# Kernel tuning notes

Measured on AMD Instinct MI355X. Metric: run time of the kernel, lower is better.

The kernel has to match this reference:

```python
import jax, jax.numpy as jnp
import numpy as np

E = 8          # moe_expert_count
CAPACITY = 1024  # per-expert capacity C = S / E (capacity factor 1)


def _top1_gate(features, wg):
    """Top-1 gate with capacity, returning combine_weights [S,E,C],
    dispatch_mask [S,E,C], and load-balancing aux loss (standard Switch/BASE-style gate
    matching the (l_aux, combine_weights, dispatch_mask) interface used by BaseLayer)."""
    S, M = features.shape
    logits = features @ wg                      # [S, E]
    gates = jax.nn.softmax(logits, axis=-1)     # [S, E]
    idx = jnp.argmax(gates, axis=-1)            # [S] expert assignment
    mask1 = jax.nn.one_hot(idx, E, dtype=features.dtype)  # [S, E]
    # position of each token inside its expert's buffer (0-based, order of arrival)
    locations = jnp.cumsum(mask1, axis=0) - mask1          # [S, E]
    loc = jnp.sum(locations * mask1, axis=1).astype(jnp.int32)  # [S]
    keep = (loc < CAPACITY).astype(features.dtype)          # drop overflow tokens
    mask1 = mask1 * keep[:, None]
    gate_s = jnp.sum(gates * mask1, axis=1)                 # [S] gate prob of kept tokens
    loc_oh = jax.nn.one_hot(loc, CAPACITY, dtype=features.dtype)  # [S, C]
    combine = gate_s[:, None, None] * mask1[:, :, None] * loc_oh[:, None, :]  # [S,E,C]
    dispatch = (combine > 0).astype(features.dtype)
    # load-balance aux loss: E * sum(mean_prob_e * frac_tokens_e)
    me = jnp.mean(gates, axis=0)
    ce = jnp.mean(mask1, axis=0)
    l_aux = jnp.sum(me * ce) * E
    return l_aux, combine, dispatch


def setup_inputs() -> dict:
    key = jax.random.key(0)
    k0, k1, k2, k3 = jax.random.split(key, 4)
    B, T, M, H = 4, 2048, 512, 1024
    return {
        "hidden_states": jax.random.normal(k0, (B, T, M), dtype=jnp.float32),
        "wg": jax.random.normal(k1, (M, E), dtype=jnp.float32) * 0.02,
        "w1": jax.random.normal(k2, (E, M, H), dtype=jnp.float32) * 0.02,
        "b1": jnp.zeros((E, H), dtype=jnp.float32),
        "w2": jax.random.normal(k3, (E, H, M), dtype=jnp.float32) * 0.02,
        "b2": jnp.zeros((E, M), dtype=jnp.float32),
    }


def reference(hidden_states, wg, w1, b1, w2, b2):
    B, T, M = hidden_states.shape
    feats = hidden_states.reshape(-1, M)            # [S, M]
    l_aux, combine, dispatch = _top1_gate(feats, wg)
    # dense one-hot dispatch matmul: (E*C, S) @ (S, M) -> [E, C, M]
    dispatched = jnp.einsum('sec,sm->ecm', dispatch, feats)
    # per-expert FFN (BaseSublayer: Linear -> ReLU -> Linear)
    h = jax.nn.relu(jnp.einsum('ecm,emh->ech', dispatched, w1) + b1[:, None, :])
    expert_out = jnp.einsum('ech,ehn->ecn', h, w2) + b2[:, None, :]  # [E, C, M]
    # dense combine matmul: (S, E*C) @ (E*C, M) -> [S, M]
    combined = jnp.einsum('sec,ecn->sn', combine, expert_out)
    return combined.reshape(B, T, -1), l_aux
```

## Files before the change

kernel.cpp:

```cpp
#include <hip/hip_runtime.h>

#define S_TOK 8192
#define M_DIM 512
#define E_NUM 8
#define CAP   1024
#define H_DIM 1024
#define NGATE_BLK (S_TOK / 4)

typedef __attribute__((ext_vector_type(8))) short bf16x8;
typedef __attribute__((ext_vector_type(4))) float f32x4;

__device__ static inline unsigned short f2bf(float f) {
    unsigned int u = __float_as_uint(f);
    unsigned int r = (u + 0x7fffu + ((u >> 16) & 1u)) >> 16;
    return (unsigned short)r;
}

__device__ static inline void async_copy16(const void* g, void* l) {
    __builtin_amdgcn_global_load_lds(
        (const __attribute__((address_space(1))) void*)g,
        (__attribute__((address_space(3))) void*)l, 16, 0, 0);
}

__global__ __launch_bounds__(256) void gate_kernel(
    const float* __restrict__ feats, const float* __restrict__ wg,
    int* __restrict__ idx, float* __restrict__ gate_top,
    float* __restrict__ gates_psum, unsigned short* __restrict__ xb)
{
    __shared__ float gsh[4][8];
    const int wave = threadIdx.x >> 6;
    const int lane = threadIdx.x & 63;
    const int s = blockIdx.x * 4 + wave;

    const float* xrow = feats + (size_t)s * M_DIM;
    const int m0 = lane * 8;

    const float4 va = *(const float4*)(xrow + m0);
    const float4 vb = *(const float4*)(xrow + m0 + 4);
    float xv[8] = {va.x, va.y, va.z, va.w, vb.x, vb.y, vb.z, vb.w};

    {
        bf16x8 o;
#pragma unroll
        for (int j = 0; j < 8; ++j) o[j] = (short)f2bf(xv[j]);
        *(bf16x8*)(xb + (size_t)s * M_DIM + m0) = o;
        if (blockIdx.x == 0 && wave == 0) {
            bf16x8 z = (bf16x8){0,0,0,0,0,0,0,0};
            *(bf16x8*)(xb + (size_t)S_TOK * M_DIM + m0) = z;
        }
    }

    float p[8];
#pragma unroll
    for (int e = 0; e < 8; ++e) p[e] = 0.f;
#pragma unroll
    for (int j = 0; j < 8; ++j) {
        const float4 wa = *(const float4*)(wg + (m0 + j) * 8);
        const float4 wb2 = *(const float4*)(wg + (m0 + j) * 8 + 4);
        const float x = xv[j];
        p[0] += x * wa.x;  p[1] += x * wa.y;  p[2] += x * wa.z;  p[3] += x * wa.w;
        p[4] += x * wb2.x; p[5] += x * wb2.y; p[6] += x * wb2.z; p[7] += x * wb2.w;
    }
#pragma unroll
    for (int e = 0; e < 8; ++e) {
        float v = p[e];
#pragma unroll
        for (int off = 1; off < 64; off <<= 1) v += __shfl_xor(v, off, 64);
        p[e] = v;
    }
    if (lane == 0) {
        float mx = p[0];
#pragma unroll
        for (int e = 1; e < 8; ++e) mx = fmaxf(mx, p[e]);
        float ex[8], sum = 0.f;
#pragma unroll
        for (int e = 0; e < 8; ++e) { ex[e] = expf(p[e] - mx); sum += ex[e]; }
        const float inv = 1.0f / sum;
        int best = 0; float bl = p[0];
#pragma unroll
        for (int e = 1; e < 8; ++e) { if (p[e] > bl) { bl = p[e]; best = e; } }
#pragma unroll
        for (int e = 0; e < 8; ++e) gsh[wave][e] = ex[e] * inv;
        idx[s] = best;
        gate_top[s] = ex[best] * inv;
    }
    __syncthreads();
    if (threadIdx.x < 8) {
        const int e = threadIdx.x;
        gates_psum[blockIdx.x * 8 + e] =
            gsh[0][e] + gsh[1][e] + gsh[2][e] + gsh[3][e];
    }
}

__global__ __launch_bounds__(256) void scan_kernel(
    const int* __restrict__ idx, const float* __restrict__ gate_top,
    const float* __restrict__ gates_psum,
    float* __restrict__ gate_final, int* __restrict__ token_list,
    int* __restrict__ kept, float* __restrict__ out)
{
    __shared__ int   cnts[256][9];
    __shared__ float wpart[4][8];
    __shared__ int   totals[8];
    __shared__ int   sdrop[7168];
    __shared__ int   dropctr;

    const int t = threadIdx.x;
    const int wv = t >> 6, ln = t & 63;
    const int base = t * 32;

    for (int i = t; i < E_NUM * CAP; i += 256) token_list[i] = S_TOK;
    if (t == 0) dropctr = 0;

    int c[8];
#pragma unroll
    for (int e = 0; e < 8; ++e) c[e] = 0;
    for (int i = 0; i < 32; ++i) {
        const int ei = idx[base + i];
#pragma unroll
        for (int e = 0; e < 8; ++e) c[e] += (ei == e) ? 1 : 0;
    }
    float g[8];
#pragma unroll
    for (int e = 0; e < 8; ++e) g[e] = 0.f;
    for (int i = 0; i < NGATE_BLK / 256; ++i) {
        const float* gp = gates_psum + (size_t)(t + 256 * i) * 8;
        const float4 a = *(const float4*)gp;
        const float4 b = *(const float4*)(gp + 4);
        g[0] += a.x; g[1] += a.y; g[2] += a.z; g[3] += a.w;
        g[4] += b.x; g[5] += b.y; g[6] += b.z; g[7] += b.w;
    }
#pragma unroll
    for (int e = 0; e < 8; ++e) cnts[t][e] = c[e];
#pragma unroll
    for (int e = 0; e < 8; ++e) {
        float v = g[e];
#pragma unroll
        for (int off = 1; off < 64; off <<= 1) v += __shfl_xor(v, off, 64);
        if (ln == 0) wpart[wv][e] = v;
    }
    __syncthreads();

#pragma unroll
    for (int ee = 0; ee < 2; ++ee) {
        const int e = wv * 2 + ee;
        int off = 0;
#pragma unroll
        for (int seg = 0; seg < 4; ++seg) {
            const int r = seg * 64 + ln;
            const int v = cnts[r][e];
            int incl = v;
#pragma unroll
            for (int d = 1; d < 64; d <<= 1) {
                const int nn = __shfl_up(incl, d, 64);
                if (ln >= d) incl += nn;
            }
            cnts[r][e] = incl - v + off;
            off += __shfl(incl, 63, 64);
        }
        if (ln == 0) {
            totals[e] = off;
            kept[e] = off < CAP ? off : CAP;
        }
    }
    __syncthreads();

    if (t == 0) {
        float l = 0.f;
        for (int e = 0; e < 8; ++e) {
            const float ms = wpart[0][e] + wpart[1][e] + wpart[2][e] + wpart[3][e];
            const int ke = totals[e] < CAP ? totals[e] : CAP;
            l += (ms / (float)S_TOK) * ((float)ke / (float)S_TOK);
        }
        out[(size_t)S_TOK * M_DIM] = l * (float)E_NUM;
    }

    int rc[8];
#pragma unroll
    for (int e = 0; e < 8; ++e) rc[e] = cnts[t][e];

    for (int i = 0; i < 32; ++i) {
        const int s = base + i;
        const int ei = idx[s];
        int loc = 0;
#pragma unroll
        for (int e = 0; e < 8; ++e) {
            if (ei == e) { loc = rc[e]; rc[e] = rc[e] + 1; }
        }
        const bool keepit = loc < CAP;
        gate_final[s] = keepit ? gate_top[s] : 0.f;
        if (keepit) {
            token_list[ei * CAP + loc] = s;
        } else {
            const int d = atomicAdd(&dropctr, 1);
            sdrop[d] = s;
        }
    }
    __syncthreads();

    const int nd = dropctr;
    for (int d = 0; d < nd; ++d) {
        const int s = sdrop[d];
        *(float2*)(out + (size_t)s * M_DIM + t * 2) = make_float2(0.f, 0.f);
    }
}

__global__ __launch_bounds__(256) void convert_w(
    const float* __restrict__ w1, unsigned short* __restrict__ w1t,
    const float* __restrict__ w2, unsigned short* __restrict__ w2t)
{
    __shared__ float tile[32][33];
    int b = blockIdx.x;
    const float* src; unsigned short* dst;
    int e, k0, n0, K, N;
    if (b < 4096) {
        e = b >> 9; k0 = ((b >> 5) & 15) * 32; n0 = (b & 31) * 32;
        K = 512; N = 1024; src = w1; dst = w1t;
    } else {
        b -= 4096;
        e = b >> 9; k0 = ((b >> 4) & 31) * 32; n0 = (b & 15) * 32;
        K = 1024; N = 512; src = w2; dst = w2t;
    }
    const int t = threadIdx.x;
    const int r = t >> 3, c4 = (t & 7) * 4;
    {
        const float4 v = *(const float4*)(src + ((size_t)e * K + k0 + r) * N + n0 + c4);
        tile[r][c4 + 0] = v.x; tile[r][c4 + 1] = v.y;
        tile[r][c4 + 2] = v.z; tile[r][c4 + 3] = v.w;
    }
    __syncthreads();
    {
        ushort4 o;
        o.x = f2bf(tile[c4 + 0][r]); o.y = f2bf(tile[c4 + 1][r]);
        o.z = f2bf(tile[c4 + 2][r]); o.w = f2bf(tile[c4 + 3][r]);
        *(ushort4*)(dst + ((size_t)e * N + n0 + r) * K + k0 + c4) = o;
    }
}

__global__ __launch_bounds__(256) void ffn1_mfma(
    const unsigned short* __restrict__ xb, const unsigned short* __restrict__ w1t,
    const float* __restrict__ b1, const int* __restrict__ tok,
    const int* __restrict__ kept, unsigned short* __restrict__ h)
{
    const int b = blockIdx.x;
    const int e = b & 7;
    const int r = b >> 3;
    const int ct = r >> 3, nt = r & 7;
    const int c0 = ct * 128, n0 = nt * 128;
    if (c0 >= kept[e]) return;

    __shared__ __align__(16) short Alds[2][128 * 64];
    __shared__ __align__(16) short Blds[2][128 * 64];
    __shared__ int srow[128];

    const int t = threadIdx.x;
    const int wave = t >> 6, lane = t & 63;
    const int wm = wave & 1, wn = wave >> 1;
    const int q = lane >> 4, lr = lane & 15;

    if (t < 128) srow[t] = tok[e * CAP + c0 + t];

    auto stage = [&](int buf, int kb) {
#pragma unroll
        for (int i = 0; i < 4; ++i) {
            const int lin = (i * 4 + wave) * 64 + lane;
            const int row = lin >> 3;
            const int ch = (lin & 7) ^ (row & 7);
            async_copy16(xb + (size_t)srow[row] * M_DIM + kb + ch * 8,
                         &Alds[buf][lin * 8]);
        }
#pragma unroll
        for (int i = 0; i < 4; ++i) {
            const int lin = (i * 4 + wave) * 64 + lane;
            const int row = lin >> 3;
            const int ch = (lin & 7) ^ (row & 7);
            async_copy16(w1t + ((size_t)e * H_DIM + n0 + row) * M_DIM + kb + ch * 8,
                         &Blds[buf][lin * 8]);
        }
    };

    f32x4 acc[4][4];
#pragma unroll
    for (int mi = 0; mi < 4; ++mi)
#pragma unroll
        for (int ni = 0; ni < 4; ++ni) acc[mi][ni] = (f32x4){0.f, 0.f, 0.f, 0.f};

    __syncthreads();
    stage(0, 0);

    int cur = 0;
    for (int kb = 0; kb < M_DIM; kb += 64) {
        __syncthreads();
        if (kb + 64 < M_DIM) stage(cur ^ 1, kb + 64);

#pragma unroll
        for (int kk = 0; kk < 64; kk += 32) {
            const int cb = kk >> 3;
            bf16x8 af[4], bfv[4];
#pragma unroll
            for (int mi = 0; mi < 4; ++mi) {
                const int R = wm * 64 + mi * 16 + lr;
                af[mi] = *(const bf16x8*)(&Alds[cur][(R * 8 + ((cb + q) ^ (R & 7))) * 8]);
            }
#pragma unroll
            for (int ni = 0; ni < 4; ++ni) {
                const int R = wn * 64 + ni * 16 + lr;
                bfv[ni] = *(const bf16x8*)(&Blds[cur][(R * 8 + ((cb + q) ^ (R & 7))) * 8]);
            }
#pragma unroll
            for (int mi = 0; mi < 4; ++mi)
#pragma unroll
                for (int ni = 0; ni < 4; ++ni)
                    acc[mi][ni] = __builtin_amdgcn_mfma_f32_16x16x32_bf16(
                        af[mi], bfv[ni], acc[mi][ni], 0, 0, 0);
        }
        cur ^= 1;
    }

#pragma unroll
    for (int ni = 0; ni < 4; ++ni) {
        const int col = n0 + wn * 64 + ni * 16 + lr;
        const float bias = b1[e * H_DIM + col];
#pragma unroll
        for (int mi = 0; mi < 4; ++mi) {
            const int rowl = wm * 64 + mi * 16 + q * 4;
            const size_t basep = (size_t)(e * CAP + c0 + rowl) * H_DIM + col;
#pragma unroll
            for (int r2 = 0; r2 < 4; ++r2) {
                const float v = fmaxf(acc[mi][ni][r2] + bias, 0.f);
                h[basep + (size_t)r2 * H_DIM] = f2bf(v);
            }
        }
    }
}

__global__ __launch_bounds__(256) void ffn2_mfma(
    const unsigned short* __restrict__ h, const unsigned short* __restrict__ w2t,
    const float* __restrict__ b2, const int* __restrict__ tok,
    const int* __restrict__ kept, const float* __restrict__ gate_final,
    float* __restrict__ out)
{
    const int b = blockIdx.x;
    const int e = b & 7;
    const int r = b >> 3;
    const int ct = r >> 3, nt = r & 7;
    const int c0 = ct * 64, n0 = nt * 64;
    if (c0 >= kept[e]) return;

    __shared__ __align__(16) short Alds[64 * 64];
    __shared__ __align__(16) short Blds[64 * 64];
    __shared__ int   stok[64];
    __shared__ float sgf[64];

    const int t = threadIdx.x;
    const int wave = t >> 6, lane = t & 63;
    const int wm = wave & 1, wn = wave >> 1;
    const int q = lane >> 4, lr = lane & 15;

    if (t < 64) {
        const int tk = tok[e * CAP + c0 + t];
        stok[t] = tk;
        sgf[t] = (tk != S_TOK) ? gate_final[tk] : 0.f;
    }

    f32x4 acc[2][2];
#pragma unroll
    for (int mi = 0; mi < 2; ++mi)
#pragma unroll
        for (int ni = 0; ni < 2; ++ni) acc[mi][ni] = (f32x4){0.f, 0.f, 0.f, 0.f};

    for (int kb = 0; kb < H_DIM; kb += 64) {
        __syncthreads();
#pragma unroll
        for (int i = 0; i < 2; ++i) {
            const int lin = (i * 4 + wave) * 64 + lane;
            const int row = lin >> 3;
            const int ch = (lin & 7) ^ (row & 7);
            async_copy16(h + (size_t)(e * CAP + c0 + row) * H_DIM + kb + ch * 8,
                         &Alds[lin * 8]);
        }
#pragma unroll
        for (int i = 0; i < 2; ++i) {
            const int lin = (i * 4 + wave) * 64 + lane;
            const int row = lin >> 3;
            const int ch = (lin & 7) ^ (row & 7);
            async_copy16(w2t + ((size_t)e * M_DIM + n0 + row) * H_DIM + kb + ch * 8,
                         &Blds[lin * 8]);
        }
        __syncthreads();

#pragma unroll
        for (int kk = 0; kk < 64; kk += 32) {
            const int cb = kk >> 3;
            bf16x8 af[2], bfv[2];
#pragma unroll
            for (int mi = 0; mi < 2; ++mi) {
                const int R = wm * 32 + mi * 16 + lr;
                af[mi] = *(const bf16x8*)(&Alds[(R * 8 + ((cb + q) ^ (R & 7))) * 8]);
            }
#pragma unroll
            for (int ni = 0; ni < 2; ++ni) {
                const int R = wn * 32 + ni * 16 + lr;
                bfv[ni] = *(const bf16x8*)(&Blds[(R * 8 + ((cb + q) ^ (R & 7))) * 8]);
            }
#pragma unroll
            for (int mi = 0; mi < 2; ++mi)
#pragma unroll
                for (int ni = 0; ni < 2; ++ni)
                    acc[mi][ni] = __builtin_amdgcn_mfma_f32_16x16x32_bf16(
                        af[mi], bfv[ni], acc[mi][ni], 0, 0, 0);
        }
    }

#pragma unroll
    for (int ni = 0; ni < 2; ++ni) {
        const int col = n0 + wn * 32 + ni * 16 + lr;
        const float bias = b2[e * M_DIM + col];
#pragma unroll
        for (int mi = 0; mi < 2; ++mi) {
            const int rowl = wm * 32 + mi * 16 + q * 4;
#pragma unroll
            for (int r2 = 0; r2 < 4; ++r2) {
                const int slot = rowl + r2;
                const int tokid = stok[slot];
                if (tokid != S_TOK) {
                    out[(size_t)tokid * M_DIM + col] = sgf[slot] * (acc[mi][ni][r2] + bias);
                }
            }
        }
    }
}

extern "C" void kernel_launch(void* const* d_in, const int* in_sizes, int n_in,
                              void* d_out, int out_size, void* d_ws, size_t ws_size,
                              hipStream_t stream) {
    const float* feats = (const float*)d_in[0];
    const float* wg    = (const float*)d_in[1];
    const float* w1    = (const float*)d_in[2];
    const float* b1    = (const float*)d_in[3];
    const float* w2    = (const float*)d_in[4];
    const float* b2    = (const float*)d_in[5];
    float* out = (float*)d_out;

    char* ws = (char*)d_ws;
    size_t off = 0;
    unsigned short* h   = (unsigned short*)(ws + off); off += (size_t)E_NUM * CAP * H_DIM * 2;
    unsigned short* xb  = (unsigned short*)(ws + off); off += (size_t)(S_TOK + 1) * M_DIM * 2;
    unsigned short* w1t = (unsigned short*)(ws + off); off += (size_t)E_NUM * H_DIM * M_DIM * 2;
    unsigned short* w2t = (unsigned short*)(ws + off); off += (size_t)E_NUM * M_DIM * H_DIM * 2;
    int*   idx        = (int*)(ws + off);   off += (size_t)S_TOK * 4;
    float* gate_top   = (float*)(ws + off); off += (size_t)S_TOK * 4;
    float* gate_final = (float*)(ws + off); off += (size_t)S_TOK * 4;
    float* gates_psum = (float*)(ws + off); off += (size_t)NGATE_BLK * 8 * 4;
    int*   token_list = (int*)(ws + off);   off += (size_t)S_TOK * 4;
    int*   kept       = (int*)(ws + off);   off += 64;
    (void)ws_size; (void)n_in; (void)in_sizes;

    gate_kernel<<<NGATE_BLK, 256, 0, stream>>>(feats, wg, idx, gate_top,
                                               gates_psum, xb);
    convert_w<<<8192, 256, 0, stream>>>(w1, w1t, w2, w2t);
    scan_kernel<<<1, 256, 0, stream>>>(idx, gate_top, gates_psum, gate_final,
                                       token_list, kept, out);
    ffn1_mfma<<<512, 256, 0, stream>>>(xb, w1t, b1, token_list, kept, h);
    ffn2_mfma<<<1024, 256, 0, stream>>>(h, w2t, b2, token_list, kept,
                                        gate_final, out);
}
```

Measured before the change: 180.6 us.

## Merge gate and weight-convert kernels; shrink ffn1 tile and drop double buffering

The gate kernel and the weight conversion/transpose kernel become one launch by splitting on block index, which removes one kernel launch and its serialization gap. ffn1 switches from 128x128 to 128x64 output tiles, doubling the grid to 1024 blocks, and drops LDS double buffering in favour of a single buffer with load-then-sync. Both FFN kernels gain a min-blocks-per-CU launch bound of 4 to raise occupancy. The cost is that async loads no longer overlap with MFMA inside a block, and each A tile is now reloaded for twice as many N tiles.

```diff
diff --git a/kernel.cpp b/kernel.cpp
--- a/kernel.cpp
+++ b/kernel.cpp
@@ -22,73 +22,105 @@
         (__attribute__((address_space(3))) void*)l, 16, 0, 0);
 }
 
-__global__ __launch_bounds__(256) void gate_kernel(
+__global__ __launch_bounds__(256) void prep_kernel(
     const float* __restrict__ feats, const float* __restrict__ wg,
     int* __restrict__ idx, float* __restrict__ gate_top,
-    float* __restrict__ gates_psum, unsigned short* __restrict__ xb)
+    float* __restrict__ gates_psum, unsigned short* __restrict__ xb,
+    const float* __restrict__ w1, unsigned short* __restrict__ w1t,
+    const float* __restrict__ w2, unsigned short* __restrict__ w2t)
 {
     __shared__ float gsh[4][8];
-    const int wave = threadIdx.x >> 6;
-    const int lane = threadIdx.x & 63;
-    const int s = blockIdx.x * 4 + wave;
-
-    const float* xrow = feats + (size_t)s * M_DIM;
-    const int m0 = lane * 8;
-
-    const float4 va = *(const float4*)(xrow + m0);
-    const float4 vb = *(const float4*)(xrow + m0 + 4);
-    float xv[8] = {va.x, va.y, va.z, va.w, vb.x, vb.y, vb.z, vb.w};
-
-    {
-        bf16x8 o;
-#pragma unroll
-        for (int j = 0; j < 8; ++j) o[j] = (short)f2bf(xv[j]);
-        *(bf16x8*)(xb + (size_t)s * M_DIM + m0) = o;
-        if (blockIdx.x == 0 && wave == 0) {
-            bf16x8 z = (bf16x8){0,0,0,0,0,0,0,0};
-            *(bf16x8*)(xb + (size_t)S_TOK * M_DIM + m0) = z;
-        }
-    }
-
-    float p[8];
-#pragma unroll
-    for (int e = 0; e < 8; ++e) p[e] = 0.f;
-#pragma unroll
-    for (int j = 0; j < 8; ++j) {
-        const float4 wa = *(const float4*)(wg + (m0 + j) * 8);
-        const float4 wb2 = *(const float4*)(wg + (m0 + j) * 8 + 4);
-        const float x = xv[j];
-        p[0] += x * wa.x;  p[1] += x * wa.y;  p[2] += x * wa.z;  p[3] += x * wa.w;
-        p[4] += x * wb2.x; p[5] += x * wb2.y; p[6] += x * wb2.z; p[7] += x * wb2.w;
-    }
-#pragma unroll
-    for (int e = 0; e < 8; ++e) {
-        float v = p[e];
-#pragma unroll
-        for (int off = 1; off < 64; off <<= 1) v += __shfl_xor(v, off, 64);
-        p[e] = v;
-    }
-    if (lane == 0) {
-        float mx = p[0];
-#pragma unroll
-        for (int e = 1; e < 8; ++e) mx = fmaxf(mx, p[e]);
-        float ex[8], sum = 0.f;
-#pragma unroll
-        for (int e = 0; e < 8; ++e) { ex[e] = expf(p[e] - mx); sum += ex[e]; }
-        const float inv = 1.0f / sum;
-        int best = 0; float bl = p[0];
-#pragma unroll
-        for (int e = 1; e < 8; ++e) { if (p[e] > bl) { bl = p[e]; best = e; } }
-#pragma unroll
-        for (int e = 0; e < 8; ++e) gsh[wave][e] = ex[e] * inv;
-        idx[s] = best;
-        gate_top[s] = ex[best] * inv;
-    }
-    __syncthreads();
-    if (threadIdx.x < 8) {
-        const int e = threadIdx.x;
-        gates_psum[blockIdx.x * 8 + e] =
-            gsh[0][e] + gsh[1][e] + gsh[2][e] + gsh[3][e];
+    __shared__ float tile[32][33];
+
+    if (blockIdx.x < NGATE_BLK) {
+        const int wave = threadIdx.x >> 6;
+        const int lane = threadIdx.x & 63;
+        const int s = blockIdx.x * 4 + wave;
+
+        const float* xrow = feats + (size_t)s * M_DIM;
+        const int m0 = lane * 8;
+
+        const float4 va = *(const float4*)(xrow + m0);
+        const float4 vb = *(const float4*)(xrow + m0 + 4);
+        float xv[8] = {va.x, va.y, va.z, va.w, vb.x, vb.y, vb.z, vb.w};
+
+        {
+            bf16x8 o;
+#pragma unroll
+            for (int j = 0; j < 8; ++j) o[j] = (short)f2bf(xv[j]);
+            *(bf16x8*)(xb + (size_t)s * M_DIM + m0) = o;
+            if (blockIdx.x == 0 && wave == 0) {
+                bf16x8 z = (bf16x8){0,0,0,0,0,0,0,0};
+                *(bf16x8*)(xb + (size_t)S_TOK * M_DIM + m0) = z;
+            }
+        }
+
+        float p[8];
+#pragma unroll
+        for (int e = 0; e < 8; ++e) p[e] = 0.f;
+#pragma unroll
+        for (int j = 0; j < 8; ++j) {
+            const float4 wa = *(const float4*)(wg + (m0 + j) * 8);
+            const float4 wb2 = *(const float4*)(wg + (m0 + j) * 8 + 4);
+            const float x = xv[j];
+            p[0] += x * wa.x;  p[1] += x * wa.y;  p[2] += x * wa.z;  p[3] += x * wa.w;
+            p[4] += x * wb2.x; p[5] += x * wb2.y; p[6] += x * wb2.z; p[7] += x * wb2.w;
+        }
+#pragma unroll
+        for (int e = 0; e < 8; ++e) {
+            float v = p[e];
+#pragma unroll
+            for (int off = 1; off < 64; off <<= 1) v += __shfl_xor(v, off, 64);
+            p[e] = v;
+        }
+        if (lane == 0) {
+            float mx = p[0];
+#pragma unroll
+            for (int e = 1; e < 8; ++e) mx = fmaxf(mx, p[e]);
+            float ex[8], sum = 0.f;
+#pragma unroll
+            for (int e = 0; e < 8; ++e) { ex[e] = expf(p[e] - mx); sum += ex[e]; }
+            const float inv = 1.0f / sum;
+            int best = 0; float bl = p[0];
+#pragma unroll
+            for (int e = 1; e < 8; ++e) { if (p[e] > bl) { bl = p[e]; best = e; } }
+#pragma unroll
+            for (int e = 0; e < 8; ++e) gsh[wave][e] = ex[e] * inv;
+            idx[s] = best;
+            gate_top[s] = ex[best] * inv;
+        }
+        __syncthreads();
+        if (threadIdx.x < 8) {
+            const int e = threadIdx.x;
+            gates_psum[blockIdx.x * 8 + e] =
+                gsh[0][e] + gsh[1][e] + gsh[2][e] + gsh[3][e];
+        }
+    } else {
+        int b = blockIdx.x - NGATE_BLK;
+        const float* src; unsigned short* dst;
+        int e, k0, n0, K, N;
+        if (b < 4096) {
+            e = b >> 9; k0 = ((b >> 5) & 15) * 32; n0 = (b & 31) * 32;
+            K = 512; N = 1024; src = w1; dst = w1t;
+        } else {
+            b -= 4096;
+            e = b >> 9; k0 = ((b >> 4) & 31) * 32; n0 = (b & 15) * 32;
+            K = 1024; N = 512; src = w2; dst = w2t;
+        }
+        const int t = threadIdx.x;
+        const int r = t >> 3, c4 = (t & 7) * 4;
+        {
+            const float4 v = *(const float4*)(src + ((size_t)e * K + k0 + r) * N + n0 + c4);
+            tile[r][c4 + 0] = v.x; tile[r][c4 + 1] = v.y;
+            tile[r][c4 + 2] = v.z; tile[r][c4 + 3] = v.w;
+        }
+        __syncthreads();
+        {
+            ushort4 o;
+            o.x = f2bf(tile[c4 + 0][r]); o.y = f2bf(tile[c4 + 1][r]);
+            o.z = f2bf(tile[c4 + 2][r]); o.w = f2bf(tile[c4 + 3][r]);
+            *(ushort4*)(dst + ((size_t)e * N + n0 + r) * K + k0 + c4) = o;
+        }
     }
 }
 
@@ -204,39 +236,7 @@
     }
 }
 
-__global__ __launch_bounds__(256) void convert_w(
-    const float* __restrict__ w1, unsigned short* __restrict__ w1t,
-    const float* __restrict__ w2, unsigned short* __restrict__ w2t)
-{
-    __shared__ float tile[32][33];
-    int b = blockIdx.x;
-    const float* src; unsigned short* dst;
-    int e, k0, n0, K, N;
-    if (b < 4096) {
-        e = b >> 9; k0 = ((b >> 5) & 15) * 32; n0 = (b & 31) * 32;
-        K = 512; N = 1024; src = w1; dst = w1t;
-    } else {
-        b -= 4096;
-        e = b >> 9; k0 = ((b >> 4) & 31) * 32; n0 = (b & 15) * 32;
-        K = 1024; N = 512; src = w2; dst = w2t;
-    }
-    const int t = threadIdx.x;
-    const int r = t >> 3, c4 = (t & 7) * 4;
-    {
-        const float4 v = *(const float4*)(src + ((size_t)e * K + k0 + r) * N + n0 + c4);
-        tile[r][c4 + 0] = v.x; tile[r][c4 + 1] = v.y;
-        tile[r][c4 + 2] = v.z; tile[r][c4 + 3] = v.w;
-    }
-    __syncthreads();
-    {
-        ushort4 o;
-        o.x = f2bf(tile[c4 + 0][r]); o.y = f2bf(tile[c4 + 1][r]);
-        o.z = f2bf(tile[c4 + 2][r]); o.w = f2bf(tile[c4 + 3][r]);
-        *(ushort4*)(dst + ((size_t)e * N + n0 + r) * K + k0 + c4) = o;
-    }
-}
-
-__global__ __launch_bounds__(256) void ffn1_mfma(
+__global__ __launch_bounds__(256, 4) void ffn1_mfma(
     const unsigned short* __restrict__ xb, const unsigned short* __restrict__ w1t,
     const float* __restrict__ b1, const int* __restrict__ tok,
     const int* __restrict__ kept, unsigned short* __restrict__ h)
@@ -244,12 +244,12 @@
     const int b = blockIdx.x;
     const int e = b & 7;
     const int r = b >> 3;
-    const int ct = r >> 3, nt = r & 7;
-    const int c0 = ct * 128, n0 = nt * 128;
+    const int ct = r >> 4, nt = r & 15;
+    const int c0 = ct * 128, n0 = nt * 64;
     if (c0 >= kept[e]) return;
 
-    __shared__ __align__(16) short Alds[2][128 * 64];
-    __shared__ __align__(16) short Blds[2][128 * 64];
+    __shared__ __align__(16) short Alds[128 * 64];
+    __shared__ __align__(16) short Blds[64 * 64];
     __shared__ int srow[128];
 
     const int t = threadIdx.x;
@@ -258,67 +258,60 @@
     const int q = lane >> 4, lr = lane & 15;
 
     if (t < 128) srow[t] = tok[e * CAP + c0 + t];
-
-    auto stage = [&](int buf, int kb) {
+    __syncthreads();
+
+    f32x4 acc[4][2];
+#pragma unroll
+    for (int mi = 0; mi < 4; ++mi)
+#pragma unroll
+        for (int ni = 0; ni < 2; ++ni) acc[mi][ni] = (f32x4){0.f, 0.f, 0.f, 0.f};
+
+    for (int kb = 0; kb < M_DIM; kb += 64) {
+        __syncthreads();
 #pragma unroll
         for (int i = 0; i < 4; ++i) {
             const int lin = (i * 4 + wave) * 64 + lane;
             const int row = lin >> 3;
             const int ch = (lin & 7) ^ (row & 7);
             async_copy16(xb + (size_t)srow[row] * M_DIM + kb + ch * 8,
-                         &Alds[buf][lin * 8]);
-        }
-#pragma unroll
-        for (int i = 0; i < 4; ++i) {
+                         &Alds[lin * 8]);
+        }
+#pragma unroll
+        for (int i = 0; i < 2; ++i) {
             const int lin = (i * 4 + wave) * 64 + lane;
             const int row = lin >> 3;
             const int ch = (lin & 7) ^ (row & 7);
             async_copy16(w1t + ((size_t)e * H_DIM + n0 + row) * M_DIM + kb + ch * 8,
-                         &Blds[buf][lin * 8]);
-        }
-    };
-
-    f32x4 acc[4][4];
-#pragma unroll
-    for (int mi = 0; mi < 4; ++mi)
-#pragma unroll
-        for (int ni = 0; ni < 4; ++ni) acc[mi][ni] = (f32x4){0.f, 0.f, 0.f, 0.f};
-
-    __syncthreads();
-    stage(0, 0);
-
-    int cur = 0;
-    for (int kb = 0; kb < M_DIM; kb += 64) {
-        __syncthreads();
-        if (kb + 64 < M_DIM) stage(cur ^ 1, kb + 64);
+                         &Blds[lin * 8]);
+        }
+        __syncthreads();
 
 #pragma unroll
         for (int kk = 0; kk < 64; kk += 32) {
             const int cb = kk >> 3;
-            bf16x8 af[4], bfv[4];
+            bf16x8 af[4], bfv[2];
 #pragma unroll
             for (int mi = 0; mi < 4; ++mi) {
                 const int R = wm * 64 + mi * 16 + lr;
-                af[mi] = *(const bf16x8*)(&Alds[cur][(R * 8 + ((cb + q) ^ (R & 7))) * 8]);
-            }
-#pragma unroll
-            for (int ni = 0; ni < 4; ++ni) {
-                const int R = wn * 64 + ni * 16 + lr;
-                bfv[ni] = *(const bf16x8*)(&Blds[cur][(R * 8 + ((cb + q) ^ (R & 7))) * 8]);
+                af[mi] = *(const bf16x8*)(&Alds[(R * 8 + ((cb + q) ^ (R & 7))) * 8]);
+            }
+#pragma unroll
+            for (int ni = 0; ni < 2; ++ni) {
+                const int R = wn * 32 + ni * 16 + lr;
+                bfv[ni] = *(const bf16x8*)(&Blds[(R * 8 + ((cb + q) ^ (R & 7))) * 8]);
             }
 #pragma unroll
             for (int mi = 0; mi < 4; ++mi)
 #pragma unroll
-                for (int ni = 0; ni < 4; ++ni)
+                for (int ni = 0; ni < 2; ++ni)
                     acc[mi][ni] = __builtin_amdgcn_mfma_f32_16x16x32_bf16(
                         af[mi], bfv[ni], acc[mi][ni], 0, 0, 0);
         }
-        cur ^= 1;
-    }
-
-#pragma unroll
-    for (int ni = 0; ni < 4; ++ni) {
-        const int col = n0 + wn * 64 + ni * 16 + lr;
+    }
+
+#pragma unroll
+    for (int ni = 0; ni < 2; ++ni) {
+        const int col = n0 + wn * 32 + ni * 16 + lr;
         const float bias = b1[e * H_DIM + col];
 #pragma unroll
         for (int mi = 0; mi < 4; ++mi) {
@@ -333,7 +326,7 @@
     }
 }
 
-__global__ __launch_bounds__(256) void ffn2_mfma(
+__global__ __launch_bounds__(256, 4) void ffn2_mfma(
     const unsigned short* __restrict__ h, const unsigned short* __restrict__ w2t,
     const float* __restrict__ b2, const int* __restrict__ tok,
     const int* __restrict__ kept, const float* __restrict__ gate_final,
@@ -455,12 +448,11 @@
     int*   kept       = (int*)(ws + off);   off += 64;
     (void)ws_size; (void)n_in; (void)in_sizes;
 
-    gate_kernel<<<NGATE_BLK, 256, 0, stream>>>(feats, wg, idx, gate_top,
-                                               gates_psum, xb);
-    convert_w<<<8192, 256, 0, stream>>>(w1, w1t, w2, w2t);
+    prep_kernel<<<NGATE_BLK + 8192, 256, 0, stream>>>(
+        feats, wg, idx, gate_top, gates_psum, xb, w1, w1t, w2, w2t);
     scan_kernel<<<1, 256, 0, stream>>>(idx, gate_top, gates_psum, gate_final,
                                        token_list, kept, out);
-    ffn1_mfma<<<512, 256, 0, stream>>>(xb, w1t, b1, token_list, kept, h);
+    ffn1_mfma<<<1024, 256, 0, stream>>>(xb, w1t, b1, token_list, kept, h);
     ffn2_mfma<<<1024, 256, 0, stream>>>(h, w2t, b2, token_list, kept,
                                         gate_final, out);
 }
```

After: 179.5 us. Within noise of the previous version (-0.6%).
